# Kernel optimization log

Measured on AMD Instinct MI355X. Metric: run time of the kernel, lower is better.

## Reference

```python
import jax, jax.numpy as jnp
import numpy as np

EMB = 1024
HEADS = 16
B, N = 2, 2048

def setup_inputs() -> dict:
    key = jax.random.key(0)
    ks = jax.random.split(key, 9)
    s = 1.0 / np.sqrt(EMB)
    return {
        "x": jax.random.normal(ks[0], (B, N, EMB), dtype=jnp.float32),
        "Wq": jax.random.normal(ks[1], (EMB, EMB), dtype=jnp.float32) * s,
        "bq": jax.random.normal(ks[2], (EMB,), dtype=jnp.float32) * 0.01,
        "Wk": jax.random.normal(ks[3], (EMB, EMB), dtype=jnp.float32) * s,
        "bk": jax.random.normal(ks[4], (EMB,), dtype=jnp.float32) * 0.01,
        "Wv": jax.random.normal(ks[5], (EMB, EMB), dtype=jnp.float32) * s,
        "bv": jax.random.normal(ks[6], (EMB,), dtype=jnp.float32) * 0.01,
        "Wo": jax.random.normal(ks[7], (EMB, EMB), dtype=jnp.float32) * s,
        "bo": jax.random.normal(ks[8], (EMB,), dtype=jnp.float32) * 0.01,
    }

def _split_heads(t):
    b, n, e = t.shape
    return t.reshape(b, n, HEADS, e // HEADS).transpose(0, 2, 1, 3)  # b h n d

def reference(x, Wq, bq, Wk, bk, Wv, bv, Wo, bo):
    q = _split_heads(x @ Wq + bq)
    k = _split_heads(x @ Wk + bk)
    v = _split_heads(x @ Wv + bv)
    # NOTE: original scales by sqrt(emb_size), not sqrt(head_dim)
    scaling = jnp.asarray(EMB, x.dtype) ** 0.5
    energy = jnp.einsum('bhqd,bhkd->bhqk', q, k)
    att = jax.nn.softmax(energy / scaling, axis=-1)
    out = jnp.einsum('bhqk,bhkd->bhqd', att, v)
    out = out.transpose(0, 2, 1, 3).reshape(x.shape[0], x.shape[1], EMB)
    return out @ Wo + bo
```

## Files before the change

### kernel.cpp

```cpp
#include <hip/hip_runtime.h>
#include <hip/hip_bf16.h>

typedef __bf16 bf16_t;
typedef bf16_t bf16x4 __attribute__((ext_vector_type(4)));
typedef bf16_t bf16x8 __attribute__((ext_vector_type(8)));
typedef float f32x4 __attribute__((ext_vector_type(4)));

#define EMB 1024
#define HEADS 16
#define BATCH 2
#define SEQ 2048
#define HD 64
#define TOKENS (BATCH * SEQ)

__device__ __forceinline__ void gld16(bf16_t* lds_dst, const bf16_t* g_src) {
    __builtin_amdgcn_global_load_lds(
        (const __attribute__((address_space(1))) unsigned int*)g_src,
        (__attribute__((address_space(3))) unsigned int*)lds_dst, 16, 0, 0);
}

__global__ __launch_bounds__(256) void convert_x(const float* __restrict__ x,
                                                 bf16_t* __restrict__ xb) {
    size_t i = ((size_t)blockIdx.x * 256 + threadIdx.x) * 16;
    f32x4 v0 = *(const f32x4*)&x[i];
    f32x4 v1 = *(const f32x4*)&x[i + 4];
    f32x4 v2 = *(const f32x4*)&x[i + 8];
    f32x4 v3 = *(const f32x4*)&x[i + 12];
    bf16x8 o0, o1;
#pragma unroll
    for (int j = 0; j < 4; ++j) {
        o0[j] = (bf16_t)v0[j]; o0[4 + j] = (bf16_t)v1[j];
        o1[j] = (bf16_t)v2[j]; o1[4 + j] = (bf16_t)v3[j];
    }
    *(bf16x8*)&xb[i] = o0;
    *(bf16x8*)&xb[i + 8] = o1;
}

__global__ __launch_bounds__(256) void prep_w(
    const float* __restrict__ W0, const float* __restrict__ W1,
    const float* __restrict__ W2, const float* __restrict__ W3,
    bf16_t* __restrict__ T0, bf16_t* __restrict__ T1,
    bf16_t* __restrict__ T2, bf16_t* __restrict__ T3) {
    __shared__ __align__(16) bf16_t T[64][72];
    int z = blockIdx.z;
    const float* src = (z == 0) ? W0 : (z == 1) ? W1 : (z == 2) ? W2 : W3;
    bf16_t* dst = (z == 0) ? T0 : (z == 1) ? T1 : (z == 2) ? T2 : T3;
    int k0 = blockIdx.y * 64, n0 = blockIdx.x * 64;
    int r = threadIdx.x >> 2, c4 = (threadIdx.x & 3) * 16;
    f32x4 v[4];
#pragma unroll
    for (int q = 0; q < 4; ++q)
        v[q] = *(const f32x4*)&src[(size_t)(k0 + r) * 1024 + n0 + c4 + q * 4];
#pragma unroll
    for (int j = 0; j < 16; ++j) T[c4 + j][r] = (bf16_t)v[j >> 2][j & 3];
    __syncthreads();
    bf16x8 o0 = *(const bf16x8*)&T[r][c4];
    bf16x8 o1 = *(const bf16x8*)&T[r][c4 + 8];
    *(bf16x8*)&dst[(size_t)(n0 + r) * 1024 + k0 + c4] = o0;
    *(bf16x8*)&dst[(size_t)(n0 + r) * 1024 + k0 + c4 + 8] = o1;
}

template <typename TO>
__global__ __launch_bounds__(256) void gemm64(
    const bf16_t* __restrict__ A,
    const bf16_t* __restrict__ Wt0, const bf16_t* __restrict__ Wt1, const bf16_t* __restrict__ Wt2,
    const float* __restrict__ b0, const float* __restrict__ b1, const float* __restrict__ b2,
    TO* __restrict__ o0, TO* __restrict__ o1, TO* __restrict__ o2,
    int md0, int md1, int md2, float sc0, float sc1, float sc2) {
    __shared__ __align__(16) bf16_t As[64 * 32];
    __shared__ __align__(16) bf16_t Bs[128 * 32];

    const int tid = threadIdx.x, w = tid >> 6, lane = tid & 63;
    const int quad = lane >> 4, c = lane & 15;
    const int wm = (w >> 1) * 32, wn = (w & 1) * 64;
    const int m0 = blockIdx.y * 64, n0 = blockIdx.x * 128;

    const int z = blockIdx.z;
    const bf16_t* W = (z == 0) ? Wt0 : (z == 1) ? Wt1 : Wt2;
    const float* bias = (z == 0) ? b0 : (z == 1) ? b1 : b2;
    TO* out = (z == 0) ? o0 : (z == 1) ? o1 : o2;
    const int mode = (z == 0) ? md0 : (z == 1) ? md1 : md2;
    const float scale = (z == 0) ? sc0 : (z == 1) ? sc1 : sc2;

    f32x4 acc[2][4];
#pragma unroll
    for (int i = 0; i < 2; ++i)
#pragma unroll
        for (int j = 0; j < 4; ++j) acc[i][j] = (f32x4){0.f, 0.f, 0.f, 0.f};

    const int srow = lane >> 2, sch = lane & 3;
    const bf16_t* Ag = A + (size_t)m0 * 1024;
    const bf16_t* Bg = W + (size_t)n0 * 1024;

    for (int k0 = 0; k0 < 1024; k0 += 32) {
        __syncthreads();
        gld16(&As[(w * 16) * 32], &Ag[(size_t)(w * 16 + srow) * 1024 + k0 + sch * 8]);
#pragma unroll
        for (int s = 0; s < 2; ++s) {
            int rg = w * 32 + s * 16;
            gld16(&Bs[rg * 32], &Bg[(size_t)(rg + srow) * 1024 + k0 + sch * 8]);
        }
        __syncthreads();

        bf16x8 af[2], bfv[4];
#pragma unroll
        for (int t = 0; t < 2; ++t)
            af[t] = *(const bf16x8*)&As[(wm + t * 16 + c) * 32 + quad * 8];
#pragma unroll
        for (int t = 0; t < 4; ++t)
            bfv[t] = *(const bf16x8*)&Bs[(wn + t * 16 + c) * 32 + quad * 8];
#pragma unroll
        for (int mt = 0; mt < 2; ++mt)
#pragma unroll
            for (int nt = 0; nt < 4; ++nt)
                acc[mt][nt] = __builtin_amdgcn_mfma_f32_16x16x32_bf16(
                    af[mt], bfv[nt], acc[mt][nt], 0, 0, 0);
    }

#pragma unroll
    for (int nt = 0; nt < 4; ++nt) {
        int col = n0 + wn + nt * 16 + c;
        float bv = bias[col];
#pragma unroll
        for (int mt = 0; mt < 2; ++mt)
#pragma unroll
            for (int r = 0; r < 4; ++r) {
                int row = m0 + wm + mt * 16 + quad * 4 + r;
                float v = (acc[mt][nt][r] + bv) * scale;
                size_t idx;
                if (mode == 0) {
                    idx = (size_t)row * 1024 + col;
                } else {
                    int bb = row >> 11, n = row & 2047;
                    int hh = col >> 6, d = col & 63;
                    idx = (mode == 1) ? ((size_t)(bb * HEADS + hh) * SEQ + n) * HD + d
                                      : ((size_t)(bb * HEADS + hh) * HD + d) * SEQ + n;
                }
                out[idx] = (TO)v;
            }
    }
}

__global__ __launch_bounds__(256) void attn_kernel(
    const bf16_t* __restrict__ Q, const bf16_t* __restrict__ K,
    const bf16_t* __restrict__ Vt, bf16_t* __restrict__ O) {
    __shared__ __align__(16) bf16_t Ks[128 * 64];
    __shared__ __align__(16) bf16_t Vs[64 * 128];
    __shared__ __align__(16) bf16_t Ps[4][2][16][72];
    __shared__ float Lbuf[2][2][64];

    const int tid = threadIdx.x, w = tid >> 6, lane = tid & 63;
    const int quad = lane >> 4, c = lane & 15;
    const int qh = w & 1, kh = w >> 1;
    const int bh = blockIdx.x, b = bh >> 4, h = bh & 15;
    const int q0 = blockIdx.y * 64;

    const bf16_t* Qg = Q + ((size_t)bh * SEQ + q0) * HD;
    bf16x8 qf[2][2];
#pragma unroll
    for (int u = 0; u < 2; ++u)
#pragma unroll
        for (int ks = 0; ks < 2; ++ks)
            qf[u][ks] = *(const bf16x8*)&Qg[(qh * 32 + u * 16 + c) * 64 + ks * 32 + quad * 8];

    f32x4 Oacc[2][4];
#pragma unroll
    for (int u = 0; u < 2; ++u)
#pragma unroll
        for (int t = 0; t < 4; ++t) Oacc[u][t] = (f32x4){0.f, 0.f, 0.f, 0.f};
    float lp[2] = {0.f, 0.f};

    const int kr = lane >> 3, kch = lane & 7;
    const int vr = lane >> 4, vch = lane & 15;

    const bf16_t* Kg = K + (size_t)bh * SEQ * HD;
    const bf16_t* Vg = Vt + (size_t)bh * HD * SEQ;

    bf16x8 kbuf[4], vbuf[4];
    auto load_tile = [&](int j0) {
#pragma unroll
        for (int s = 0; s < 4; ++s) {
            int krow = w * 32 + s * 8 + kr;
            kbuf[s] = *(const bf16x8*)&Kg[(size_t)(j0 + krow) * 64 + (kch ^ kr) * 8];
            int vrow = w * 16 + s * 4 + vr;
            vbuf[s] = *(const bf16x8*)&Vg[(size_t)vrow * SEQ + j0 + (vch ^ (vrow & 15)) * 8];
        }
    };
    load_tile(0);

    for (int j0 = 0; j0 < SEQ; j0 += 128) {
        __syncthreads();
#pragma unroll
        for (int s = 0; s < 4; ++s) {
            int krow = w * 32 + s * 8 + kr;
            *(bf16x8*)&Ks[krow * 64 + kch * 8] = kbuf[s];
            int vrow = w * 16 + s * 4 + vr;
            *(bf16x8*)&Vs[vrow * 128 + vch * 8] = vbuf[s];
        }
        __syncthreads();
        if (j0 + 128 < SEQ) load_tile(j0 + 128);

        f32x4 S[2][4];
#pragma unroll
        for (int u = 0; u < 2; ++u)
#pragma unroll
            for (int t = 0; t < 4; ++t) S[u][t] = (f32x4){0.f, 0.f, 0.f, 0.f};
#pragma unroll
        for (int ks = 0; ks < 2; ++ks)
#pragma unroll
            for (int t = 0; t < 4; ++t) {
                int row = kh * 64 + t * 16 + c;
                bf16x8 kv = *(const bf16x8*)&Ks[row * 64 + (((ks * 4 + quad) ^ (c & 7)) * 8)];
                S[0][t] = __builtin_amdgcn_mfma_f32_16x16x32_bf16(kv, qf[0][ks], S[0][t], 0, 0, 0);
                S[1][t] = __builtin_amdgcn_mfma_f32_16x16x32_bf16(kv, qf[1][ks], S[1][t], 0, 0, 0);
            }

#pragma unroll
        for (int u = 0; u < 2; ++u)
#pragma unroll
            for (int t = 0; t < 4; ++t) {
                bf16x4 pk;
#pragma unroll
                for (int r = 0; r < 4; ++r) {
                    float p = __builtin_amdgcn_exp2f(S[u][t][r]);
                    lp[u] += p;
                    pk[r] = (bf16_t)p;
                }
                *(bf16x4*)&Ps[w][u][c][t * 16 + quad * 4] = pk;
            }

#pragma unroll
        for (int ks2 = 0; ks2 < 2; ++ks2) {
            bf16x8 af0 = *(const bf16x8*)&Ps[w][0][c][ks2 * 32 + quad * 8];
            bf16x8 af1 = *(const bf16x8*)&Ps[w][1][c][ks2 * 32 + quad * 8];
#pragma unroll
            for (int t = 0; t < 4; ++t) {
                int row = t * 16 + c;
                bf16x8 vv = *(const bf16x8*)&Vs[row * 128 + (((kh * 8 + ks2 * 4 + quad) ^ c) * 8)];
                Oacc[0][t] = __builtin_amdgcn_mfma_f32_16x16x32_bf16(af0, vv, Oacc[0][t], 0, 0, 0);
                Oacc[1][t] = __builtin_amdgcn_mfma_f32_16x16x32_bf16(af1, vv, Oacc[1][t], 0, 0, 0);
            }
        }
    }

#pragma unroll
    for (int u = 0; u < 2; ++u) {
        lp[u] += __shfl_xor(lp[u], 16);
        lp[u] += __shfl_xor(lp[u], 32);
    }

    __syncthreads();
    float* Obuf = (float*)Ks;
    if (kh == 1) {
#pragma unroll
        for (int u = 0; u < 2; ++u) {
#pragma unroll
            for (int t = 0; t < 4; ++t)
                *(f32x4*)&Obuf[(((qh * 2 + u) * 4 + t) * 64 + lane) * 4] = Oacc[u][t];
            Lbuf[qh][u][lane] = lp[u];
        }
    }
    __syncthreads();
    if (kh == 0) {
        float lr[2][4];
#pragma unroll
        for (int u = 0; u < 2; ++u) {
            lp[u] += Lbuf[qh][u][lane];
#pragma unroll
            for (int r = 0; r < 4; ++r) lr[u][r] = __shfl(lp[u], quad * 4 + r);
        }
#pragma unroll
        for (int u = 0; u < 2; ++u)
#pragma unroll
            for (int t = 0; t < 4; ++t) {
                f32x4 part = *(const f32x4*)&Obuf[(((qh * 2 + u) * 4 + t) * 64 + lane) * 4];
#pragma unroll
                for (int r = 0; r < 4; ++r) {
                    int qrow = q0 + qh * 32 + u * 16 + quad * 4 + r;
                    size_t idx = ((size_t)(b * SEQ + qrow)) * EMB + h * 64 + t * 16 + c;
                    O[idx] = (bf16_t)((Oacc[u][t][r] + part[r]) / lr[u][r]);
                }
            }
    }
}

extern "C" void kernel_launch(void* const* d_in, const int* in_sizes, int n_in,
                              void* d_out, int out_size, void* d_ws, size_t ws_size,
                              hipStream_t stream) {
    (void)in_sizes; (void)n_in; (void)out_size; (void)ws_size;
    const float* x  = (const float*)d_in[0];
    const float* Wq = (const float*)d_in[1];
    const float* bq = (const float*)d_in[2];
    const float* Wk = (const float*)d_in[3];
    const float* bk = (const float*)d_in[4];
    const float* Wv = (const float*)d_in[5];
    const float* bv = (const float*)d_in[6];
    const float* Wo = (const float*)d_in[7];
    const float* bo = (const float*)d_in[8];

    bf16_t* ws = (bf16_t*)d_ws;
    const size_t NELEM = (size_t)TOKENS * EMB;
    const size_t WELEM = (size_t)EMB * EMB;
    bf16_t* Qb  = ws;
    bf16_t* Kb  = ws + NELEM;
    bf16_t* Vtb = ws + 2 * NELEM;
    bf16_t* Ob  = ws + 3 * NELEM;
    bf16_t* xb  = ws + 4 * NELEM;
    bf16_t* Wt0 = ws + 5 * NELEM;
    bf16_t* Wt1 = Wt0 + WELEM;
    bf16_t* Wt2 = Wt0 + 2 * WELEM;
    bf16_t* Wt3 = Wt0 + 3 * WELEM;

    const float QSCALE = 1.4426950408889634f / 32.0f;

    hipLaunchKernelGGL(convert_x, dim3(1024), dim3(256), 0, stream, x, xb);
    hipLaunchKernelGGL(prep_w, dim3(16, 16, 4), dim3(256), 0, stream,
                       Wq, Wk, Wv, Wo, Wt0, Wt1, Wt2, Wt3);
    hipLaunchKernelGGL((gemm64<bf16_t>), dim3(8, 64, 3), dim3(256), 0, stream,
                       xb, Wt0, Wt1, Wt2, bq, bk, bv, Qb, Kb, Vtb,
                       1, 1, 2, QSCALE, 1.0f, 1.0f);
    hipLaunchKernelGGL(attn_kernel, dim3(32, 32), dim3(256), 0, stream, Qb, Kb, Vtb, Ob);
    hipLaunchKernelGGL((gemm64<float>), dim3(8, 64, 1), dim3(256), 0, stream,
                       Ob, Wt3, Wt3, Wt3, bo, bo, bo,
                       (float*)d_out, (float*)d_out, (float*)d_out,
                       0, 0, 0, 1.0f, 1.0f, 1.0f);
}
```

Measured before the change: 231.7 us.

## Fuse QKV projections into one GEMM sharing A tiles; prefetch O-proj via registers

```diff
diff --git a/kernel.cpp b/kernel.cpp
--- a/kernel.cpp
+++ b/kernel.cpp
@@ -60,47 +60,127 @@
     *(bf16x8*)&dst[(size_t)(n0 + r) * 1024 + k0 + c4 + 8] = o1;
 }
 
-template <typename TO>
-__global__ __launch_bounds__(256) void gemm64(
+__global__ __launch_bounds__(256) void qkv_gemm(
     const bf16_t* __restrict__ A,
     const bf16_t* __restrict__ Wt0, const bf16_t* __restrict__ Wt1, const bf16_t* __restrict__ Wt2,
-    const float* __restrict__ b0, const float* __restrict__ b1, const float* __restrict__ b2,
-    TO* __restrict__ o0, TO* __restrict__ o1, TO* __restrict__ o2,
-    int md0, int md1, int md2, float sc0, float sc1, float sc2) {
+    const float* __restrict__ bq, const float* __restrict__ bk, const float* __restrict__ bv,
+    bf16_t* __restrict__ Qb, bf16_t* __restrict__ Kb, bf16_t* __restrict__ Vtb,
+    float qscale) {
     __shared__ __align__(16) bf16_t As[64 * 32];
-    __shared__ __align__(16) bf16_t Bs[128 * 32];
+    __shared__ __align__(16) bf16_t Bs[3][128 * 32];
 
     const int tid = threadIdx.x, w = tid >> 6, lane = tid & 63;
     const int quad = lane >> 4, c = lane & 15;
     const int wm = (w >> 1) * 32, wn = (w & 1) * 64;
     const int m0 = blockIdx.y * 64, n0 = blockIdx.x * 128;
 
-    const int z = blockIdx.z;
-    const bf16_t* W = (z == 0) ? Wt0 : (z == 1) ? Wt1 : Wt2;
-    const float* bias = (z == 0) ? b0 : (z == 1) ? b1 : b2;
-    TO* out = (z == 0) ? o0 : (z == 1) ? o1 : o2;
-    const int mode = (z == 0) ? md0 : (z == 1) ? md1 : md2;
-    const float scale = (z == 0) ? sc0 : (z == 1) ? sc1 : sc2;
-
-    f32x4 acc[2][4];
-#pragma unroll
-    for (int i = 0; i < 2; ++i)
-#pragma unroll
-        for (int j = 0; j < 4; ++j) acc[i][j] = (f32x4){0.f, 0.f, 0.f, 0.f};
+    f32x4 acc[3][2][4];
+#pragma unroll
+    for (int i = 0; i < 3; ++i)
+#pragma unroll
+        for (int mt = 0; mt < 2; ++mt)
+#pragma unroll
+            for (int nt = 0; nt < 4; ++nt) acc[i][mt][nt] = (f32x4){0.f, 0.f, 0.f, 0.f};
 
     const int srow = lane >> 2, sch = lane & 3;
     const bf16_t* Ag = A + (size_t)m0 * 1024;
-    const bf16_t* Bg = W + (size_t)n0 * 1024;
+    const bf16_t* Bg[3] = {Wt0 + (size_t)n0 * 1024, Wt1 + (size_t)n0 * 1024,
+                           Wt2 + (size_t)n0 * 1024};
 
     for (int k0 = 0; k0 < 1024; k0 += 32) {
         __syncthreads();
         gld16(&As[(w * 16) * 32], &Ag[(size_t)(w * 16 + srow) * 1024 + k0 + sch * 8]);
 #pragma unroll
-        for (int s = 0; s < 2; ++s) {
-            int rg = w * 32 + s * 16;
-            gld16(&Bs[rg * 32], &Bg[(size_t)(rg + srow) * 1024 + k0 + sch * 8]);
-        }
-        __syncthreads();
+        for (int i = 0; i < 3; ++i)
+#pragma unroll
+            for (int s = 0; s < 2; ++s) {
+                int rg = w * 32 + s * 16;
+                gld16(&Bs[i][rg * 32], &Bg[i][(size_t)(rg + srow) * 1024 + k0 + sch * 8]);
+            }
+        __syncthreads();
+
+        bf16x8 af[2];
+#pragma unroll
+        for (int t = 0; t < 2; ++t)
+            af[t] = *(const bf16x8*)&As[(wm + t * 16 + c) * 32 + quad * 8];
+#pragma unroll
+        for (int i = 0; i < 3; ++i) {
+#pragma unroll
+            for (int nt = 0; nt < 4; ++nt) {
+                bf16x8 bfv = *(const bf16x8*)&Bs[i][(wn + nt * 16 + c) * 32 + quad * 8];
+#pragma unroll
+                for (int mt = 0; mt < 2; ++mt)
+                    acc[i][mt][nt] = __builtin_amdgcn_mfma_f32_16x16x32_bf16(
+                        af[mt], bfv, acc[i][mt][nt], 0, 0, 0);
+            }
+        }
+    }
+
+#pragma unroll
+    for (int i = 0; i < 3; ++i) {
+        const float* bias = (i == 0) ? bq : (i == 1) ? bk : bv;
+        const float scale = (i == 0) ? qscale : 1.0f;
+#pragma unroll
+        for (int nt = 0; nt < 4; ++nt) {
+            int col = n0 + wn + nt * 16 + c;
+            float bvv = bias[col];
+            int hh = col >> 6, d = col & 63;
+#pragma unroll
+            for (int mt = 0; mt < 2; ++mt)
+#pragma unroll
+                for (int r = 0; r < 4; ++r) {
+                    int row = m0 + wm + mt * 16 + quad * 4 + r;
+                    int bb = row >> 11, n = row & 2047;
+                    float v = (acc[i][mt][nt][r] + bvv) * scale;
+                    if (i == 2) {
+                        Vtb[((size_t)(bb * HEADS + hh) * HD + d) * SEQ + n] = (bf16_t)v;
+                    } else {
+                        bf16_t* dst = (i == 0) ? Qb : Kb;
+                        dst[((size_t)(bb * HEADS + hh) * SEQ + n) * HD + d] = (bf16_t)v;
+                    }
+                }
+        }
+    }
+}
+
+__global__ __launch_bounds__(256) void oproj_gemm(
+    const bf16_t* __restrict__ A, const bf16_t* __restrict__ Wt,
+    const float* __restrict__ bias, float* __restrict__ out) {
+    __shared__ __align__(16) bf16_t As[64 * 32];
+    __shared__ __align__(16) bf16_t Bs[128 * 32];
+
+    const int tid = threadIdx.x, w = tid >> 6, lane = tid & 63;
+    const int quad = lane >> 4, c = lane & 15;
+    const int wm = (w >> 1) * 32, wn = (w & 1) * 64;
+    const int m0 = blockIdx.y * 64, n0 = blockIdx.x * 128;
+
+    f32x4 acc[2][4];
+#pragma unroll
+    for (int i = 0; i < 2; ++i)
+#pragma unroll
+        for (int j = 0; j < 4; ++j) acc[i][j] = (f32x4){0.f, 0.f, 0.f, 0.f};
+
+    const int srow = lane >> 2, sch = lane & 3;
+    const bf16_t* Ag = A + (size_t)m0 * 1024;
+    const bf16_t* Bg = Wt + (size_t)n0 * 1024;
+
+    bf16x8 abuf, bbuf[2];
+    auto load_tile = [&](int k0) {
+        abuf = *(const bf16x8*)&Ag[(size_t)(w * 16 + srow) * 1024 + k0 + sch * 8];
+#pragma unroll
+        for (int s = 0; s < 2; ++s)
+            bbuf[s] = *(const bf16x8*)&Bg[(size_t)(w * 32 + s * 16 + srow) * 1024 + k0 + sch * 8];
+    };
+    load_tile(0);
+
+    for (int k0 = 0; k0 < 1024; k0 += 32) {
+        __syncthreads();
+        *(bf16x8*)&As[(w * 16 + srow) * 32 + sch * 8] = abuf;
+#pragma unroll
+        for (int s = 0; s < 2; ++s)
+            *(bf16x8*)&Bs[(w * 32 + s * 16 + srow) * 32 + sch * 8] = bbuf[s];
+        __syncthreads();
+        if (k0 + 32 < 1024) load_tile(k0 + 32);
 
         bf16x8 af[2], bfv[4];
 #pragma unroll
@@ -126,17 +206,7 @@
 #pragma unroll
             for (int r = 0; r < 4; ++r) {
                 int row = m0 + wm + mt * 16 + quad * 4 + r;
-                float v = (acc[mt][nt][r] + bv) * scale;
-                size_t idx;
-                if (mode == 0) {
-                    idx = (size_t)row * 1024 + col;
-                } else {
-                    int bb = row >> 11, n = row & 2047;
-                    int hh = col >> 6, d = col & 63;
-                    idx = (mode == 1) ? ((size_t)(bb * HEADS + hh) * SEQ + n) * HD + d
-                                      : ((size_t)(bb * HEADS + hh) * HD + d) * SEQ + n;
-                }
-                out[idx] = (TO)v;
+                out[(size_t)row * 1024 + col] = acc[mt][nt][r] + bv;
             }
     }
 }
@@ -316,12 +386,9 @@
     hipLaunchKernelGGL(convert_x, dim3(1024), dim3(256), 0, stream, x, xb);
     hipLaunchKernelGGL(prep_w, dim3(16, 16, 4), dim3(256), 0, stream,
                        Wq, Wk, Wv, Wo, Wt0, Wt1, Wt2, Wt3);
-    hipLaunchKernelGGL((gemm64<bf16_t>), dim3(8, 64, 3), dim3(256), 0, stream,
-                       xb, Wt0, Wt1, Wt2, bq, bk, bv, Qb, Kb, Vtb,
-                       1, 1, 2, QSCALE, 1.0f, 1.0f);
+    hipLaunchKernelGGL(qkv_gemm, dim3(8, 64), dim3(256), 0, stream,
+                       xb, Wt0, Wt1, Wt2, bq, bk, bv, Qb, Kb, Vtb, QSCALE);
     hipLaunchKernelGGL(attn_kernel, dim3(32, 32), dim3(256), 0, stream, Qb, Kb, Vtb, Ob);
-    hipLaunchKernelGGL((gemm64<float>), dim3(8, 64, 1), dim3(256), 0, stream,
-                       Ob, Wt3, Wt3, Wt3, bo, bo, bo,
-                       (float*)d_out, (float*)d_out, (float*)d_out,
-                       0, 0, 0, 1.0f, 1.0f, 1.0f);
-}
+    hipLaunchKernelGGL(oproj_gemm, dim3(8, 64), dim3(256), 0, stream,
+                       Ob, Wt3, bo, (float*)d_out);
+}
```

New measurement: 245.2 us. 1.06x slower.
